# Optimization experiments

Hardware: AMD Instinct MI355X
Metric: run time of the kernel (lower is better)

Reference implementation:

```python
import jax, jax.numpy as jnp
import numpy as np

K = 500        # conv kernel == stride (non-overlapping windows)
C_IN = 8       # embedding dim
C_OUT = 128    # conv out channels
VOCAB = 257    # 256 byte values + padding idx 256


def setup_inputs() -> dict:
    key = jax.random.key(0)
    ks = jax.random.split(key, 10)
    B, L = 8, 1 << 20
    x = jax.random.randint(ks[0], (B, L), 0, VOCAB, dtype=jnp.int32)
    emb = 0.1 * jax.random.normal(ks[1], (VOCAB, C_IN), jnp.float32)
    emb = emb.at[VOCAB - 1].set(0.0)  # padding_idx=256 -> zero row
    lim_c = 1.0 / np.sqrt(C_IN * K)
    w1 = jax.random.uniform(ks[2], (C_OUT, C_IN, K), jnp.float32, -lim_c, lim_c)
    b1 = jax.random.uniform(ks[3], (C_OUT,), jnp.float32, -lim_c, lim_c)
    w2 = jax.random.uniform(ks[4], (C_OUT, C_IN, K), jnp.float32, -lim_c, lim_c)
    b2 = jax.random.uniform(ks[5], (C_OUT,), jnp.float32, -lim_c, lim_c)
    lim_d = 1.0 / np.sqrt(C_OUT)
    wd1 = jax.random.uniform(ks[6], (C_OUT, C_OUT), jnp.float32, -lim_d, lim_d)
    bd1 = jax.random.uniform(ks[7], (C_OUT,), jnp.float32, -lim_d, lim_d)
    wd2 = jax.random.uniform(ks[8], (1, C_OUT), jnp.float32, -lim_d, lim_d)
    bd2 = jax.random.uniform(ks[9], (1,), jnp.float32, -lim_d, lim_d)
    return {"x": x, "emb": emb, "w1": w1, "b1": b1, "w2": w2, "b2": b2,
            "wd1": wd1, "bd1": bd1, "wd2": wd2, "bd2": bd2}


def reference(x, emb, w1, b1, w2, b2, wd1, bd1, wd2, bd2):
    B, L = x.shape
    T = (L - K) // K + 1  # valid conv output length (== L // K here)
    xe = emb[x]                                  # [B, L, 8]  embedding lookup
    win = xe[:, : T * K].reshape(B, T, K, C_IN)  # [B, T, 500, 8] non-overlap windows
    c1 = jnp.einsum('btke,oek->bto', win, w1) + b1  # [B, T, 128]
    c2 = jnp.einsum('btke,oek->bto', win, w2) + b2
    gated = jax.nn.relu(c1) * jax.nn.sigmoid(c2)    # gated activation
    pooled = jnp.max(gated, axis=1)                 # global max pool over time -> [B, 128]
    h = jax.nn.relu(pooled @ wd1.T + bd1)           # [B, 128]
    out = jax.nn.sigmoid(h @ wd2.T + bd2)           # [B, 1]
    return out
```

## Files before the change

kernel.cpp:

```cpp
#include <hip/hip_runtime.h>

#define BATCH   8
#define LSEQ    1048576
#define KCONV   500
#define TWIN    2097
#define MROWS   16776
#define KDIM    4000
#define NDIM    256
#define COUT    128
#define VOCAB   257
#define VOCABP  256

#define BMR     80
#define NTILE   210
#define SLABP   20
#define NSLAB   25
#define NG      125
#define PLANE   (NDIM * 32)
#define AROWSH  168
#define STAGEN  (BMR * SLABP)

#define WTF_OFF   0ull
#define WTF_BYTES ((size_t)NG * PLANE * 2)
#define POOL_OFF  (WTF_OFF + WTF_BYTES)

typedef __attribute__((ext_vector_type(8))) __bf16 bf16x8;
typedef __attribute__((ext_vector_type(4))) float  floatx4;

__device__ inline unsigned short f2bf(float f) {
    union { float f; unsigned u; } c; c.f = f;
    return (unsigned short)((c.u + 0x7FFFu + ((c.u >> 16) & 1u)) >> 16);
}
__device__ inline unsigned pack2(float lo, float hi) {
    return (unsigned)f2bf(lo) | ((unsigned)f2bf(hi) << 16);
}

#define LDS_BARRIER() asm volatile("s_waitcnt lgkmcnt(0)\n\ts_barrier" ::: "memory")

__global__ __launch_bounds__(256) void wprep_kernel(const float* __restrict__ w1,
                                                    const float* __restrict__ w2,
                                                    unsigned short* __restrict__ Wtf,
                                                    float* __restrict__ pool) {
    const int n   = blockIdx.x;
    const int tid = threadIdx.x;
    __shared__ float tile[KDIM];
    const float* src = (n < COUT) ? (w1 + (size_t)n * KDIM)
                                  : (w2 + (size_t)(n - COUT) * KDIM);
    for (int i = tid; i < KDIM; i += 256) tile[i] = src[i];
    __syncthreads();
    for (int i = tid; i < KDIM; i += 256) {
        int g = i >> 5, kk = i & 31;
        Wtf[(size_t)g * PLANE + n * 32 + kk] = f2bf(tile[(i & 7) * KCONV + (i >> 3)]);
    }
    if (n == 0 && tid < BATCH * COUT / 2)
        ((float2*)pool)[tid] = float2{0.f, 0.f};
}

__global__ __launch_bounds__(512) void gemm_kernel(const int* __restrict__ x,
                                                   const float* __restrict__ emb,
                                                   const unsigned short* __restrict__ Wtf,
                                                   const float* __restrict__ b1,
                                                   const float* __restrict__ b2,
                                                   float* __restrict__ pool) {
    __shared__ unsigned short tableL[VOCAB * 8];
    __shared__ unsigned short As[2][BMR * AROWSH];

    const int tid  = threadIdx.x;
    const int lane = tid & 63;
    const int wv   = tid >> 6;
    const int m0   = blockIdx.x * BMR;
    const int r16  = lane & 15;
    const int q    = lane >> 4;

    const int wg   = wv >> 2;
    const int wn   = wv & 3;
    const int ntw  = wg ? 2 : 3;
    const int tb   = wg * 3;

    if (tid < VOCAB) {
        const float4* er = (const float4*)(emb + tid * 8);
        float4 a = er[0], b = er[1];
        uint4 u;
        u.x = pack2(a.x, a.y); u.y = pack2(a.z, a.w);
        u.z = pack2(b.x, b.y); u.w = pack2(b.z, b.w);
        *(uint4*)(tableL + tid * 8) = u;
    }

    const int* xptr[4];
    int        loff[4];
    bool       sval[4];
#pragma unroll
    for (int l = 0; l < 4; ++l) {
        int idx = tid + 512 * l;
        sval[l] = (idx < STAGEN);
        int ic  = sval[l] ? idx : 0;
        int row = ic / SLABP;
        int pos = ic - row * SLABP;
        int am  = m0 + row;
        bool av = sval[l] && (am < MROWS);
        sval[l] = av;
        int amc = av ? am : 0;
        int b   = amc / TWIN;
        int t   = amc - b * TWIN;
        xptr[l] = x + ((size_t)b * LSEQ + (size_t)t * KCONV + pos);
        loff[l] = row * AROWSH + pos * 8;
    }

    const size_t bb0 = (size_t)(wn * 32 + r16) * 32 + q * 8;
    const size_t boff[4] = { bb0, bb0 + 16 * 32, bb0 + 128 * 32, bb0 + 144 * 32 };

    floatx4 acc[3][4];
#pragma unroll
    for (int i = 0; i < 3; ++i)
#pragma unroll
        for (int j = 0; j < 4; ++j) acc[i][j] = floatx4{0.f, 0.f, 0.f, 0.f};

    int xv[4], xn[4];
#pragma unroll
    for (int l = 0; l < 4; ++l) xv[l] = sval[l] ? xptr[l][0] : VOCABP;
    __syncthreads();

#pragma unroll
    for (int l = 0; l < 4; ++l) {
        if (l == 3 && tid >= STAGEN - 3 * 512) break;
        uint4 g = *(const uint4*)(tableL + xv[l] * 8);
        *(uint4*)((unsigned short*)As + loff[l]) = g;
    }
#pragma unroll
    for (int l = 0; l < 4; ++l) xv[l] = sval[l] ? xptr[l][SLABP] : VOCABP;
    LDS_BARRIER();

    bf16x8 bc0[4], bc1[4], bc2[4] = {};
#pragma unroll
    for (int j = 0; j < 4; ++j) {
        bc0[j] = *(const bf16x8*)(Wtf + boff[j]);
        bc1[j] = *(const bf16x8*)(Wtf + PLANE + boff[j]);
    }

    int buf = 0;
    for (int s = 0; s < NSLAB; ++s) {
        if (s + 2 < NSLAB) {
#pragma unroll
            for (int l = 0; l < 4; ++l)
                xn[l] = sval[l] ? xptr[l][(s + 2) * SLABP] : VOCABP;
        }

        const unsigned short* Asb = (const unsigned short*)As + buf * (BMR * AROWSH);
#pragma unroll
        for (int kt = 0; kt < 5; ++kt) {
            const int g = s * 5 + kt;
            if (g + 2 < NG) {
                const unsigned short* Wp = Wtf + (size_t)(g + 2) * PLANE;
#pragma unroll
                for (int j = 0; j < 4; ++j) bc2[j] = *(const bf16x8*)(Wp + boff[j]);
            }
            bf16x8 af[3];
#pragma unroll
            for (int i = 0; i < 3; ++i)
                if (i < ntw)
                    af[i] = *(const bf16x8*)(Asb + ((tb + i) * 16 + r16) * AROWSH + (kt * 4 + q) * 8);
#pragma unroll
            for (int i = 0; i < 3; ++i)
                if (i < ntw) {
#pragma unroll
                    for (int j = 0; j < 4; ++j)
                        acc[i][j] = __builtin_amdgcn_mfma_f32_16x16x32_bf16(af[i], bc0[j], acc[i][j], 0, 0, 0);
                }
#pragma unroll
            for (int j = 0; j < 4; ++j) { bc0[j] = bc1[j]; bc1[j] = bc2[j]; }
        }

        if (s + 1 < NSLAB) {
            unsigned short* d = (unsigned short*)As + (buf ^ 1) * (BMR * AROWSH);
#pragma unroll
            for (int l = 0; l < 4; ++l) {
                if (l == 3 && tid >= STAGEN - 3 * 512) break;
                uint4 g = *(const uint4*)(tableL + xv[l] * 8);
                *(uint4*)(d + loff[l]) = g;
            }
        }
#pragma unroll
        for (int l = 0; l < 4; ++l) xv[l] = xn[l];
        LDS_BARRIER();
        buf ^= 1;
    }

#pragma unroll
    for (int jj = 0; jj < 2; ++jj) {
        const int o = wn * 32 + jj * 16 + r16;
        const float b1v = b1[o], b2v = b2[o];
        float cur = 0.0f;
        int curb  = (m0 + tb * 16 + q * 4) / TWIN;
#pragma unroll
        for (int i = 0; i < 3; ++i) {
            if (i < ntw) {
#pragma unroll
                for (int rg = 0; rg < 4; ++rg) {
                    const int row = m0 + (tb + i) * 16 + q * 4 + rg;
                    if (row < MROWS) {
                        const int bb = row / TWIN;
                        if (bb != curb) {
                            atomicMax((int*)&pool[curb * COUT + o], __float_as_int(cur));
                            cur = 0.0f; curb = bb;
                        }
                        const float c1 = acc[i][jj][rg] + b1v;
                        const float c2 = acc[i][jj + 2][rg] + b2v;
                        const float g  = fmaxf(c1, 0.0f) / (1.0f + __expf(-c2));
                        cur = fmaxf(cur, g);
                    }
                }
            }
        }
        atomicMax((int*)&pool[curb * COUT + o], __float_as_int(cur));
    }
}

__global__ __launch_bounds__(128) void head_kernel(const float* __restrict__ pool,
                                                   const float* __restrict__ wd1,
                                                   const float* __restrict__ bd1,
                                                   const float* __restrict__ wd2,
                                                   const float* __restrict__ bd2,
                                                   float* __restrict__ out) {
    __shared__ float red[BATCH][COUT];
    int j = threadIdx.x;
    float wj = wd2[j];
#pragma unroll
    for (int b = 0; b < BATCH; ++b) {
        float s = bd1[j];
        for (int i = 0; i < COUT; ++i) s += pool[b * COUT + i] * wd1[j * COUT + i];
        red[b][j] = fmaxf(s, 0.0f) * wj;
    }
    __syncthreads();
    if (j < BATCH) {
        float s = 0.0f;
        for (int i = 0; i < COUT; ++i) s += red[j][i];
        out[j] = 1.0f / (1.0f + expf(-(s + bd2[0])));
    }
}

extern "C" void kernel_launch(void* const* d_in, const int* in_sizes, int n_in,
                              void* d_out, int out_size, void* d_ws, size_t ws_size,
                              hipStream_t stream) {
    const int*   x   = (const int*)d_in[0];
    const float* emb = (const float*)d_in[1];
    const float* w1  = (const float*)d_in[2];
    const float* b1  = (const float*)d_in[3];
    const float* w2  = (const float*)d_in[4];
    const float* b2  = (const float*)d_in[5];
    const float* wd1 = (const float*)d_in[6];
    const float* bd1 = (const float*)d_in[7];
    const float* wd2 = (const float*)d_in[8];
    const float* bd2 = (const float*)d_in[9];
    float* out = (float*)d_out;

    unsigned short* Wtf  = (unsigned short*)((char*)d_ws + WTF_OFF);
    float*          pool = (float*)((char*)d_ws + POOL_OFF);

    wprep_kernel<<<dim3(NDIM), dim3(256), 0, stream>>>(w1, w2, Wtf, pool);
    gemm_kernel<<<dim3(NTILE), dim3(512), 0, stream>>>(x, emb, Wtf, b1, b2, pool);
    head_kernel<<<dim3(1), dim3(128), 0, stream>>>(pool, wd1, bd1, wd2, bd2, out);
}
```

Baseline: 181.4 us.

## Warp-specialize GEMM block into stager waves and MFMA compute waves

Splits the 8 waves of each block into 4 stager waves, which fetch token ids and build the embedded A tile in LDS, and 4 compute waves, which each own all 5 row tiles for a 32-column slice and issue the MFMAs. Before, every wave did both jobs. The aim is to overlap gather/staging latency with matrix math. It also raises per-wave accumulator count (5x4 tiles) while asking for 2 blocks per CU via launch bounds, which risks register pressure or spills. Half the waves no longer issue MFMAs, so compute throughput now rests on fewer waves.

```diff
diff --git a/kernel.cpp b/kernel.cpp
--- a/kernel.cpp
+++ b/kernel.cpp
@@ -19,6 +19,7 @@
 #define PLANE   (NDIM * 32)
 #define AROWSH  168
 #define STAGEN  (BMR * SLABP)
+#define NSL     7
 
 #define WTF_OFF   0ull
 #define WTF_BYTES ((size_t)NG * PLANE * 2)
@@ -56,12 +57,12 @@
         ((float2*)pool)[tid] = float2{0.f, 0.f};
 }
 
-__global__ __launch_bounds__(512) void gemm_kernel(const int* __restrict__ x,
-                                                   const float* __restrict__ emb,
-                                                   const unsigned short* __restrict__ Wtf,
-                                                   const float* __restrict__ b1,
-                                                   const float* __restrict__ b2,
-                                                   float* __restrict__ pool) {
+__global__ __launch_bounds__(512, 2) void gemm_kernel(const int* __restrict__ x,
+                                                      const float* __restrict__ emb,
+                                                      const unsigned short* __restrict__ Wtf,
+                                                      const float* __restrict__ b1,
+                                                      const float* __restrict__ b2,
+                                                      float* __restrict__ pool) {
     __shared__ unsigned short tableL[VOCAB * 8];
     __shared__ unsigned short As[2][BMR * AROWSH];
 
@@ -71,11 +72,32 @@
     const int m0   = blockIdx.x * BMR;
     const int r16  = lane & 15;
     const int q    = lane >> 4;
-
-    const int wg   = wv >> 2;
-    const int wn   = wv & 3;
-    const int ntw  = wg ? 2 : 3;
-    const int tb   = wg * 3;
+    const bool stager = (wv >= 4);
+    const int tid2 = tid & 255;
+
+    const int* xptr[NSL];
+    int  loff[NSL];
+    bool wval[NSL], sval[NSL];
+    int  xv[NSL], xn[NSL];
+    if (stager) {
+#pragma unroll
+        for (int l = 0; l < NSL; ++l) {
+            int idx = tid2 + 256 * l;
+            wval[l] = (idx < STAGEN);
+            int ic  = wval[l] ? idx : 0;
+            int row = ic / SLABP;
+            int pos = ic - row * SLABP;
+            int am  = m0 + row;
+            sval[l] = wval[l] && (am < MROWS);
+            int amc = (am < MROWS) ? am : 0;
+            int b   = amc / TWIN;
+            int t   = amc - b * TWIN;
+            xptr[l] = x + ((size_t)b * LSEQ + (size_t)t * KCONV + pos);
+            loff[l] = row * AROWSH + pos * 8;
+        }
+#pragma unroll
+        for (int l = 0; l < NSL; ++l) xv[l] = sval[l] ? xptr[l][0] : VOCABP;
+    }
 
     if (tid < VOCAB) {
         const float4* er = (const float4*)(emb + tid * 8);
@@ -86,117 +108,95 @@
         *(uint4*)(tableL + tid * 8) = u;
     }
 
-    const int* xptr[4];
-    int        loff[4];
-    bool       sval[4];
-#pragma unroll
-    for (int l = 0; l < 4; ++l) {
-        int idx = tid + 512 * l;
-        sval[l] = (idx < STAGEN);
-        int ic  = sval[l] ? idx : 0;
-        int row = ic / SLABP;
-        int pos = ic - row * SLABP;
-        int am  = m0 + row;
-        bool av = sval[l] && (am < MROWS);
-        sval[l] = av;
-        int amc = av ? am : 0;
-        int b   = amc / TWIN;
-        int t   = amc - b * TWIN;
-        xptr[l] = x + ((size_t)b * LSEQ + (size_t)t * KCONV + pos);
-        loff[l] = row * AROWSH + pos * 8;
-    }
-
-    const size_t bb0 = (size_t)(wn * 32 + r16) * 32 + q * 8;
+    const size_t bb0 = (size_t)(wv * 32 + r16) * 32 + q * 8;
     const size_t boff[4] = { bb0, bb0 + 16 * 32, bb0 + 128 * 32, bb0 + 144 * 32 };
-
-    floatx4 acc[3][4];
-#pragma unroll
-    for (int i = 0; i < 3; ++i)
+    floatx4 acc[5][4];
+#pragma unroll
+    for (int i = 0; i < 5; ++i)
 #pragma unroll
         for (int j = 0; j < 4; ++j) acc[i][j] = floatx4{0.f, 0.f, 0.f, 0.f};
-
-    int xv[4], xn[4];
-#pragma unroll
-    for (int l = 0; l < 4; ++l) xv[l] = sval[l] ? xptr[l][0] : VOCABP;
+    bf16x8 bc0[4], bc1[4], bc2[4] = {};
+
     __syncthreads();
 
-#pragma unroll
-    for (int l = 0; l < 4; ++l) {
-        if (l == 3 && tid >= STAGEN - 3 * 512) break;
-        uint4 g = *(const uint4*)(tableL + xv[l] * 8);
-        *(uint4*)((unsigned short*)As + loff[l]) = g;
-    }
-#pragma unroll
-    for (int l = 0; l < 4; ++l) xv[l] = sval[l] ? xptr[l][SLABP] : VOCABP;
+    if (stager) {
+#pragma unroll
+        for (int l = 0; l < NSL; ++l) {
+            if (wval[l]) {
+                uint4 g = *(const uint4*)(tableL + xv[l] * 8);
+                *(uint4*)((unsigned short*)As + loff[l]) = g;
+            }
+        }
+#pragma unroll
+        for (int l = 0; l < NSL; ++l) xv[l] = sval[l] ? xptr[l][SLABP] : VOCABP;
+    } else {
+#pragma unroll
+        for (int j = 0; j < 4; ++j) {
+            bc0[j] = *(const bf16x8*)(Wtf + boff[j]);
+            bc1[j] = *(const bf16x8*)(Wtf + PLANE + boff[j]);
+        }
+    }
     LDS_BARRIER();
-
-    bf16x8 bc0[4], bc1[4], bc2[4] = {};
-#pragma unroll
-    for (int j = 0; j < 4; ++j) {
-        bc0[j] = *(const bf16x8*)(Wtf + boff[j]);
-        bc1[j] = *(const bf16x8*)(Wtf + PLANE + boff[j]);
-    }
 
     int buf = 0;
     for (int s = 0; s < NSLAB; ++s) {
-        if (s + 2 < NSLAB) {
-#pragma unroll
-            for (int l = 0; l < 4; ++l)
-                xn[l] = sval[l] ? xptr[l][(s + 2) * SLABP] : VOCABP;
-        }
-
-        const unsigned short* Asb = (const unsigned short*)As + buf * (BMR * AROWSH);
-#pragma unroll
-        for (int kt = 0; kt < 5; ++kt) {
-            const int g = s * 5 + kt;
-            if (g + 2 < NG) {
-                const unsigned short* Wp = Wtf + (size_t)(g + 2) * PLANE;
-#pragma unroll
-                for (int j = 0; j < 4; ++j) bc2[j] = *(const bf16x8*)(Wp + boff[j]);
-            }
-            bf16x8 af[3];
-#pragma unroll
-            for (int i = 0; i < 3; ++i)
-                if (i < ntw)
-                    af[i] = *(const bf16x8*)(Asb + ((tb + i) * 16 + r16) * AROWSH + (kt * 4 + q) * 8);
-#pragma unroll
-            for (int i = 0; i < 3; ++i)
-                if (i < ntw) {
+        if (stager) {
+            if (s + 2 < NSLAB) {
+#pragma unroll
+                for (int l = 0; l < NSL; ++l)
+                    xn[l] = sval[l] ? xptr[l][(s + 2) * SLABP] : VOCABP;
+            }
+            if (s + 1 < NSLAB) {
+                unsigned short* d = (unsigned short*)As + (buf ^ 1) * (BMR * AROWSH);
+#pragma unroll
+                for (int l = 0; l < NSL; ++l) {
+                    if (wval[l]) {
+                        uint4 g = *(const uint4*)(tableL + xv[l] * 8);
+                        *(uint4*)(d + loff[l]) = g;
+                    }
+                }
+            }
+#pragma unroll
+            for (int l = 0; l < NSL; ++l) xv[l] = xn[l];
+        } else {
+            const unsigned short* Asb = (const unsigned short*)As + buf * (BMR * AROWSH);
+#pragma unroll
+            for (int kt = 0; kt < 5; ++kt) {
+                const int g = s * 5 + kt;
+                if (g + 2 < NG) {
+                    const unsigned short* Wp = Wtf + (size_t)(g + 2) * PLANE;
+#pragma unroll
+                    for (int j = 0; j < 4; ++j) bc2[j] = *(const bf16x8*)(Wp + boff[j]);
+                }
+                bf16x8 af[5];
+#pragma unroll
+                for (int i = 0; i < 5; ++i)
+                    af[i] = *(const bf16x8*)(Asb + (i * 16 + r16) * AROWSH + (kt * 4 + q) * 8);
+#pragma unroll
+                for (int i = 0; i < 5; ++i)
 #pragma unroll
                     for (int j = 0; j < 4; ++j)
                         acc[i][j] = __builtin_amdgcn_mfma_f32_16x16x32_bf16(af[i], bc0[j], acc[i][j], 0, 0, 0);
-                }
-#pragma unroll
-            for (int j = 0; j < 4; ++j) { bc0[j] = bc1[j]; bc1[j] = bc2[j]; }
-        }
-
-        if (s + 1 < NSLAB) {
-            unsigned short* d = (unsigned short*)As + (buf ^ 1) * (BMR * AROWSH);
-#pragma unroll
-            for (int l = 0; l < 4; ++l) {
-                if (l == 3 && tid >= STAGEN - 3 * 512) break;
-                uint4 g = *(const uint4*)(tableL + xv[l] * 8);
-                *(uint4*)(d + loff[l]) = g;
-            }
-        }
-#pragma unroll
-        for (int l = 0; l < 4; ++l) xv[l] = xn[l];
+#pragma unroll
+                for (int j = 0; j < 4; ++j) { bc0[j] = bc1[j]; bc1[j] = bc2[j]; }
+            }
+        }
         LDS_BARRIER();
         buf ^= 1;
     }
 
-#pragma unroll
-    for (int jj = 0; jj < 2; ++jj) {
-        const int o = wn * 32 + jj * 16 + r16;
-        const float b1v = b1[o], b2v = b2[o];
-        float cur = 0.0f;
-        int curb  = (m0 + tb * 16 + q * 4) / TWIN;
-#pragma unroll
-        for (int i = 0; i < 3; ++i) {
-            if (i < ntw) {
+    if (!stager) {
+#pragma unroll
+        for (int jj = 0; jj < 2; ++jj) {
+            const int o = wv * 32 + jj * 16 + r16;
+            const float b1v = b1[o], b2v = b2[o];
+            float cur = 0.0f;
+            int curb  = (m0 + q * 4) / TWIN;
+#pragma unroll
+            for (int i = 0; i < 5; ++i) {
 #pragma unroll
                 for (int rg = 0; rg < 4; ++rg) {
-                    const int row = m0 + (tb + i) * 16 + q * 4 + rg;
+                    const int row = m0 + i * 16 + q * 4 + rg;
                     if (row < MROWS) {
                         const int bb = row / TWIN;
                         if (bb != curb) {
@@ -210,8 +210,8 @@
                     }
                 }
             }
-        }
-        atomicMax((int*)&pool[curb * COUT + o], __float_as_int(cur));
+            atomicMax((int*)&pool[curb * COUT + o], __float_as_int(cur));
+        }
     }
 }
 
```

New measurement: 180.8 us. No clear change (-0.3%).
